# Kernel tuning notes

Measured on AMD Instinct MI355X. Metric: run time of the kernel, lower is better.

The kernel has to match this reference:

```python
import jax, jax.numpy as jnp
import numpy as np

OBS, ACT, H, B = 128, 32, 64, 32768
TMAX = 8  # max variable-length GRU steps: (15-1)//2+1 == 15//2+1 == 8
CENTER = 7


def gru_last(x_seq, valid, Wih, Whh, bih, bhh):
    """torch nn.GRU cell, masked scan; returns final hidden at each true length.
    x_seq: (B, TMAX, D), valid: (B, TMAX) bool. Gate order r, z, n."""
    Bn = x_seq.shape[0]
    h0 = jnp.zeros((Bn, Whh.shape[1]), x_seq.dtype)

    def step(h, inp):
        xt, vt = inp  # (B, D), (B,)
        gi = xt @ Wih.T + bih
        gh = h @ Whh.T + bhh
        ir, iz, inn = jnp.split(gi, 3, axis=-1)
        hr, hz, hn = jnp.split(gh, 3, axis=-1)
        r = jax.nn.sigmoid(ir + hr)
        zg = jax.nn.sigmoid(iz + hz)
        n = jnp.tanh(inn + r * hn)
        hnew = (1.0 - zg) * n + zg * h
        h = jnp.where(vt[:, None], hnew, h)
        return h, None

    h, _ = jax.lax.scan(step, h0, (jnp.swapaxes(x_seq, 0, 1), valid.T))
    return h


def setup_inputs() -> dict:
    key = jax.random.key(0)
    ks = jax.random.split(key, 20)
    def p(k, shape, s=0.05):
        return jax.random.normal(k, shape, jnp.float32) * s
    D = OBS + ACT
    return dict(
        obs_chunk=jax.random.normal(ks[0], (B, 15, OBS), jnp.float32),
        act_chunk=jax.random.normal(ks[1], (B, 15, ACT), jnp.float32),
        ln_g=jnp.ones((3,), jnp.float32), ln_b=jnp.zeros((3,), jnp.float32),
        dw1=p(ks[2], (16, 3)), db1=jnp.zeros((16,), jnp.float32),
        dw2=p(ks[3], (8, 16)), db2=jnp.zeros((8,), jnp.float32),
        dw3=p(ks[4], (14, 8)), db3=jnp.zeros((14,), jnp.float32),
        Wih_f=p(ks[5], (3 * H, D)), Whh_f=p(ks[6], (3 * H, H)),
        bih_f=jnp.zeros((3 * H,), jnp.float32), bhh_f=jnp.zeros((3 * H,), jnp.float32),
        Wih_b=p(ks[7], (3 * H, D)), Whh_b=p(ks[8], (3 * H, H)),
        bih_b=jnp.zeros((3 * H,), jnp.float32), bhh_b=jnp.zeros((3 * H,), jnp.float32),
        mw1=p(ks[9], (H, 2 * H)), mb1=jnp.zeros((H,), jnp.float32),
        mw2=p(ks[10], (H, H)), mb2=jnp.zeros((H,), jnp.float32),
        mu_w=p(ks[11], (H, H)), mu_b=jnp.zeros((H,), jnp.float32),
        lv_w=p(ks[12], (H, H)), lv_b=jnp.zeros((H,), jnp.float32),
    )


def reference(obs_chunk, act_chunk, ln_g, ln_b, dw1, db1, dw2, db2, dw3, db3,
              Wih_f, Whh_f, bih_f, bhh_f, Wih_b, Whh_b, bih_b, bhh_b,
              mw1, mb1, mw2, mb2, mu_w, mu_b, lv_w, lv_b):
    C = CENTER
    # --- DynamicTimeWindow features ---
    obs_t = obs_chunk[:, C]  # (B, OBS)
    pr = jax.nn.softmax(obs_t, axis=-1)
    entropy = -jnp.sum(pr * jnp.log(pr + 1e-8), axis=-1, keepdims=True)
    diffs = jnp.stack([jnp.linalg.norm(obs_chunk[:, C - k] - obs_chunk[:, C - k - 1], axis=-1)
                       for k in range(3)], axis=1)
    roc = diffs.mean(axis=1, keepdims=True)
    act_prev = act_chunk[:, C - 1]
    md = max(obs_t.shape[-1], act_prev.shape[-1])
    op = jnp.pad(obs_t, ((0, 0), (0, md - obs_t.shape[-1])))
    ap = jnp.pad(act_prev, ((0, 0), (0, md - act_prev.shape[-1])))
    oc = op - op.mean(axis=1, keepdims=True)
    ac = ap - ap.mean(axis=1, keepdims=True)
    denom = (jnp.linalg.norm(oc, axis=1, keepdims=True)
             * jnp.linalg.norm(ac, axis=1, keepdims=True) + 1e-8)
    corr = jnp.sum(oc * ac, axis=1, keepdims=True) / denom
    f = jnp.concatenate([entropy, roc, corr], axis=1)  # (B, 3)
    mean = f.mean(axis=-1, keepdims=True)
    var = f.var(axis=-1, keepdims=True)  # biased, matches torch LayerNorm
    fn = (f - mean) / jnp.sqrt(var + 1e-5) * ln_g + ln_b
    h1 = jax.nn.relu(fn @ dw1.T + db1)
    h2 = jax.nn.relu(h1 @ dw2.T + db2)
    logits = h2 @ dw3.T + db3  # (B, 14)
    widx = jnp.argmax(logits, axis=1)  # test_mode: argmax of softmax == argmax of logits
    wl = widx + 2  # window_len in [2, 15]
    idxs = jnp.arange(15)[None, :]
    start = (C - (wl - 1) // 2)[:, None]
    end = (C + wl // 2 + 1)[:, None]
    mask = ((idxs >= start) & (idxs < end)).astype(obs_chunk.dtype)  # (B, 15)
    x = jnp.concatenate([obs_chunk, act_chunk], axis=-1) * mask[..., None]  # (B, 15, D)
    # --- BiGRU over variable-length windows ---
    len_f = (wl - 1) // 2 + 1  # (B,)
    len_b = wl // 2 + 1
    t = jnp.arange(TMAX)
    idx_f = C - len_f[:, None] + 1 + t[None, :]  # left-aligned forward window
    idx_b = C + len_b[:, None] - 1 - t[None, :]  # reversed backward window
    seq_f = jnp.take_along_axis(x, idx_f[..., None], axis=1)  # (B, 8, D)
    seq_b = jnp.take_along_axis(x, idx_b[..., None], axis=1)
    vf = t[None, :] < len_f[:, None]
    vb = t[None, :] < len_b[:, None]
    h_f = gru_last(seq_f, vf, Wih_f, Whh_f, bih_f, bhh_f)  # (B, H)
    h_b = gru_last(seq_b, vb, Wih_b, Whh_b, bih_b, bhh_b)
    comb = jnp.concatenate([h_f, h_b], axis=1)  # (B, 2H)
    zenc = jax.nn.relu(comb @ mw1.T + mb1) @ mw2.T + mb2
    mu = zenc @ mu_w.T + mu_b
    sigma = jnp.exp(0.5 * (zenc @ lv_w.T + lv_b))
    z = mu  # test_mode=True
    return (z, mu, sigma)
```

## Files before the change

### kernel.cpp

```cpp
#include <hip/hip_runtime.h>

#define OBS 128
#define ACTD 32
#define DIMX 160
#define HID 64
#define NBATCH 32768
#define TMAXX 8
#define CTR 7
#define NPOS 15

typedef short bf16x8 __attribute__((ext_vector_type(8)));
typedef float f32x4 __attribute__((ext_vector_type(4)));

#define MFMA(a,b,c) __builtin_amdgcn_mfma_f32_16x16x32_bf16((a),(b),(c),0,0,0)

#define CTRL_BYTE 262144
#define SIDX_BYTE 278528
#define SIDX_CAP  66048
#define WB_BYTE   542720
#define COMB_BYTE 755712
#define NCB 64
#define EPB 512
#define BB_OFF 40
#define BH_OFF (40 + 1024)
#define HEAD_W_OFF 10752
#define TOTAL_SLOTS 13312

__device__ __forceinline__ unsigned short f2bf(float f) {
  unsigned u = __float_as_uint(f);
  return (unsigned short)((u + 0x7FFFu + ((u >> 16) & 1u)) >> 16);
}
__device__ __forceinline__ unsigned cvtpk(float a, float b) {
  unsigned r;
  asm("v_cvt_pk_bf16_f32 %0, %1, %2" : "=v"(r) : "v"(a), "v"(b));
  return r;
}

__device__ __forceinline__ float wsum(float v) {
#pragma unroll
  for (int s = 1; s < 64; s <<= 1) v += __shfl_xor(v, s);
  return v;
}
__device__ __forceinline__ float wmax(float v) {
#pragma unroll
  for (int s = 1; s < 64; s <<= 1) v = fmaxf(v, __shfl_xor(v, s));
  return v;
}

__global__ __launch_bounds__(256) void k_prep(
    const float* __restrict__ Wih_f, const float* __restrict__ Whh_f,
    const float* __restrict__ Wih_b, const float* __restrict__ Whh_b,
    const float* __restrict__ mw1, const float* __restrict__ mw2,
    const float* __restrict__ mu_w, const float* __restrict__ lv_w,
    unsigned short* __restrict__ dst) {
  int slot = blockIdx.x * 256 + threadIdx.x;
  if (slot >= TOTAL_SLOTS) return;
  const float* src;
  if (slot < HEAD_W_OFF) {
    int d = slot / 5376, r = slot % 5376;
    int f = r >> 8, rw = r & 255;
    int w = rw >> 6, lane = rw & 63;
    int col = lane & 15, kgrp = lane >> 4;
    int row = 16 * w + col;
    if (f < 15) {
      int g = f / 5, kf = f % 5;
      const float* W = d ? Wih_b : Wih_f;
      src = W + (size_t)(g * 64 + row) * 160 + kf * 32 + kgrp * 8;
    } else {
      int f2 = f - 15, g = f2 >> 1, kh = f2 & 1;
      const float* W = d ? Whh_b : Whh_f;
      src = W + (size_t)(g * 64 + row) * 64 + kh * 32 + kgrp * 8;
    }
  } else {
    int s2 = slot - HEAD_W_OFF;
    int f = s2 >> 8, rw = s2 & 255;
    int w = rw >> 6, lane = rw & 63;
    int col = lane & 15, kgrp = lane >> 4;
    int gr = 16 * w + col;
    if (f < 4)      src = mw1 + (size_t)gr * 128 + f * 32 + kgrp * 8;
    else if (f < 6) src = mw2 + (size_t)gr * 64 + (f - 4) * 32 + kgrp * 8;
    else if (f < 8) src = mu_w + (size_t)gr * 64 + (f - 6) * 32 + kgrp * 8;
    else            src = lv_w + (size_t)gr * 64 + (f - 8) * 32 + kgrp * 8;
  }
  unsigned short* o = dst + (size_t)slot * 8;
#pragma unroll
  for (int i = 0; i < 8; i++) o[i] = f2bf(src[i]);
}

__global__ __launch_bounds__(256) void k_decide(
    const float* __restrict__ obs, const float* __restrict__ act,
    const float* __restrict__ ln_g, const float* __restrict__ ln_b,
    const float* __restrict__ dw1, const float* __restrict__ db1,
    const float* __restrict__ dw2, const float* __restrict__ db2,
    const float* __restrict__ dw3, const float* __restrict__ db3,
    int* __restrict__ lens) {
  int b = blockIdx.x * 4 + (threadIdx.x >> 6);
  int l = threadIdx.x & 63;
  const float* o7 = obs + ((size_t)b * NPOS + CTR) * OBS;
  const float* o6 = o7 - OBS;
  const float* o5 = o7 - 2 * OBS;
  const float* o4 = o7 - 3 * OBS;
  float x0 = o7[l], x1 = o7[l + 64];
  float y60 = o6[l], y61 = o6[l + 64];
  float y50 = o5[l], y51 = o5[l + 64];
  float y40 = o4[l], y41 = o4[l + 64];
  float ap = (l < 32) ? act[((size_t)b * NPOS + 6) * ACTD + l] : 0.0f;

  float m = wmax(fmaxf(x0, x1));
  float e0 = __expf(x0 - m), e1 = __expf(x1 - m);
  float s = wsum(e0 + e1);
  float dot = wsum(e0 * (x0 - m) + e1 * (x1 - m));
  float ent = __logf(s) - dot / s;

  float d0 = wsum((x0 - y60) * (x0 - y60) + (x1 - y61) * (x1 - y61));
  float d1 = wsum((y60 - y50) * (y60 - y50) + (y61 - y51) * (y61 - y51));
  float d2 = wsum((y50 - y40) * (y50 - y40) + (y51 - y41) * (y51 - y41));
  float roc = (sqrtf(d0) + sqrtf(d1) + sqrtf(d2)) / 3.0f;

  float sop = wsum(x0 + x1);
  float sop2 = wsum(x0 * x0 + x1 * x1);
  float sap = wsum(ap);
  float sap2 = wsum(ap * ap);
  float dotoa = wsum(ap * x0);
  float mo = sop / 128.0f, ma = sap / 128.0f;
  float num = dotoa - 128.0f * mo * ma;
  float oc2 = fmaxf(sop2 - 128.0f * mo * mo, 0.0f);
  float ac2 = fmaxf(sap2 - 128.0f * ma * ma, 0.0f);
  float corr = num / (sqrtf(oc2) * sqrtf(ac2) + 1e-8f);

  float f0 = ent, f1 = roc, f2 = corr;
  float mean = (f0 + f1 + f2) / 3.0f;
  float v0 = f0 - mean, v1 = f1 - mean, v2 = f2 - mean;
  float var = (v0 * v0 + v1 * v1 + v2 * v2) / 3.0f;
  float sd = sqrtf(var + 1e-5f);
  float fn0 = v0 / sd * ln_g[0] + ln_b[0];
  float fn1 = v1 / sd * ln_g[1] + ln_b[1];
  float fn2 = v2 / sd * ln_g[2] + ln_b[2];

  float h1[16];
#pragma unroll
  for (int i = 0; i < 16; i++) {
    float a = db1[i] + fn0 * dw1[i * 3] + fn1 * dw1[i * 3 + 1] + fn2 * dw1[i * 3 + 2];
    h1[i] = fmaxf(a, 0.0f);
  }
  float h2[8];
#pragma unroll
  for (int i = 0; i < 8; i++) {
    float a = db2[i];
#pragma unroll
    for (int j = 0; j < 16; j++) a += h1[j] * dw2[i * 16 + j];
    h2[i] = fmaxf(a, 0.0f);
  }
  float best = -3.0e38f;
  int bi = 0;
#pragma unroll
  for (int i = 0; i < 14; i++) {
    float a = db3[i];
#pragma unroll
    for (int j = 0; j < 8; j++) a += h2[j] * dw3[i * 8 + j];
    if (a > best) { best = a; bi = i; }
  }
  int wl = bi + 2;
  if (l == 0) {
    lens[b] = (wl - 1) / 2 + 1;
    lens[NBATCH + b] = wl / 2 + 1;
  }
}

__global__ __launch_bounds__(256) void k_count(
    const int* __restrict__ lens, int* __restrict__ ctrl) {
  __shared__ int hist[16];
  const int tid = threadIdx.x, blk = blockIdx.x;
  if (tid < 16) hist[tid] = 0;
  __syncthreads();
#pragma unroll
  for (int j = 0; j < 2; j++) {
    int e = blk * EPB + j * 256 + tid;
    atomicAdd(&hist[lens[e] - 1], 1);
    atomicAdd(&hist[8 + lens[NBATCH + e] - 1], 1);
  }
  __syncthreads();
  if (tid < 16) ctrl[BH_OFF + blk * 16 + tid] = hist[tid];
}

__global__ void k_scan(int* __restrict__ ctrl, int* __restrict__ sidx) {
  __shared__ int tot[16];
  __shared__ int pss[17];
  __shared__ int border[16];
  __shared__ int bstart[16];
  const int tid = threadIdx.x;
  const int* bh = ctrl + BH_OFF;
  int* bb = ctrl + BB_OFF;
  if (tid < 16) {
    int s = 0;
    for (int blk = 0; blk < NCB; blk++) {
      bb[blk * 16 + tid] = s;
      s += bh[blk * 16 + tid];
    }
    tot[tid] = s;
  }
  __syncthreads();
  if (tid == 0) {
    int acc = 0;
    for (int r = 0; r < 16; r++) {
      int bin = (r & 1) * 8 + 7 - (r >> 1);
      border[r] = bin;
      pss[r] = acc;
      bstart[bin] = acc;
      acc += (tot[bin] + 31) & ~31;
    }
    pss[16] = acc;
    for (int r = 0; r < 17; r++) ctrl[r] = pss[r];
    for (int r = 0; r < 16; r++) ctrl[17 + r] = border[r];
  }
  __syncthreads();
  if (tid < 16) {
    for (int blk = 0; blk < NCB; blk++) bb[blk * 16 + tid] += bstart[tid];
  }
  __syncthreads();
  for (int r = 0; r < 16; r++) {
    int bin = border[r];
    int s = pss[r] + tot[bin], e2 = pss[r + 1];
    for (int i = s + tid; i < e2; i += 64) sidx[i] = -1;
  }
}

__global__ __launch_bounds__(256) void k_place(
    const int* __restrict__ lens, const int* __restrict__ ctrl,
    int* __restrict__ sidx) {
  __shared__ int hist[16];
  __shared__ int base[16];
  const int tid = threadIdx.x, blk = blockIdx.x;
  if (tid < 16) {
    hist[tid] = 0;
    base[tid] = ctrl[BB_OFF + blk * 16 + tid];
  }
  __syncthreads();
#pragma unroll
  for (int j = 0; j < 2; j++) {
    int e = blk * EPB + j * 256 + tid;
    int binf = lens[e] - 1;
    sidx[base[binf] + atomicAdd(&hist[binf], 1)] = e;
    int binb = 8 + lens[NBATCH + e] - 1;
    sidx[base[binb] + atomicAdd(&hist[binb], 1)] = e;
  }
}

__global__ __launch_bounds__(256, 2) void k_gru(
    const float* __restrict__ obs, const float* __restrict__ act,
    const int* __restrict__ ctrl, const int* __restrict__ sidx,
    const unsigned short* __restrict__ wbf,
    const float* __restrict__ bih_f, const float* __restrict__ bhh_f,
    const float* __restrict__ bih_b, const float* __restrict__ bhh_b,
    unsigned short* __restrict__ comb) {
  __shared__ unsigned short Xl[2][32 * 168];
  __shared__ unsigned short Hl[2][32 * 72];
  __shared__ int ei[32];

  const int tid = threadIdx.x;
  const int p = blockIdx.x * 32;
  if (p >= ctrl[16]) return;
  int r = 0;
#pragma unroll
  for (int k = 1; k < 16; k++) r += (p >= ctrl[k]) ? 1 : 0;
  const int bin = ctrl[17 + r];
  const int d = bin >> 3;
  const int len = (bin & 7) + 1;

  if (tid < 32) ei[tid] = sidx[p + tid];
  __syncthreads();

  const int w = tid >> 6, l = tid & 63;
  const int col = l & 15, kgrp = l >> 4;
  const int gr = 16 * w + col;

  const float* bih = d ? bih_b : bih_f;
  const float* bhh = d ? bhh_b : bhh_f;
  const float bias_r = bih[gr] + bhh[gr];
  const float bias_z = bih[64 + gr] + bhh[64 + gr];
  const float bias_in = bih[128 + gr];
  const float bias_hn = bhh[128 + gr];

  const unsigned short* fb = wbf + ((size_t)d * 5376 + tid) * 8;
  bf16x8 wr[5], wz[5], wn[5];
#pragma unroll
  for (int kf = 0; kf < 5; kf++) {
    wr[kf] = *(const bf16x8*)(fb + (size_t)kf * 2048);
    wz[kf] = *(const bf16x8*)(fb + (size_t)(5 + kf) * 2048);
    wn[kf] = *(const bf16x8*)(fb + (size_t)(10 + kf) * 2048);
  }
  bf16x8 vr[2], vz[2], vn[2];
#pragma unroll
  for (int kh = 0; kh < 2; kh++) {
    vr[kh] = *(const bf16x8*)(fb + (size_t)(15 + kh) * 2048);
    vz[kh] = *(const bf16x8*)(fb + (size_t)(17 + kh) * 2048);
    vn[kh] = *(const bf16x8*)(fb + (size_t)(19 + kh) * 2048);
  }

  const int p0 = d ? (CTR + len - 1) : (CTR - len + 1);
  const float* pst[5];
  int sstr[5], sdo[5];
#pragma unroll
  for (int it = 0; it < 5; it++) {
    int i = tid + it * 256;
    int eloc = i / 40;
    int q = i - eloc * 40;
    int eg = ei[eloc];
    if (eg < 0) eg = ei[0];
    if (q < 32) {
      pst[it] = obs + ((size_t)eg * NPOS + p0) * OBS + q * 4;
      sstr[it] = d ? -OBS : OBS;
    } else {
      pst[it] = act + ((size_t)eg * NPOS + p0) * ACTD + (q - 32) * 4;
      sstr[it] = d ? -ACTD : ACTD;
    }
    sdo[it] = eloc * 168 + ((q < 32) ? q * 4 : 128 + (q - 32) * 4);
  }
  float4 sv[5];

  auto stage_issue = [&](int t1) {
#pragma unroll
    for (int it = 0; it < 5; it++)
      sv[it] = *(const float4*)(pst[it] + (ptrdiff_t)t1 * sstr[it]);
  };
  auto stage_commit = [&](int buf) {
#pragma unroll
    for (int it = 0; it < 5; it++) {
      uint2 pk;
      pk.x = cvtpk(sv[it].x, sv[it].y);
      pk.y = cvtpk(sv[it].z, sv[it].w);
      *(uint2*)(&Xl[buf][sdo[it]]) = pk;
    }
  };

  stage_issue(0);
  stage_commit(0);
  __syncthreads();

  f32x4 hreg[2];
#pragma unroll
  for (int m = 0; m < 2; m++) hreg[m] = (f32x4){0.f, 0.f, 0.f, 0.f};

  for (int t = 0; t < len; t++) {
    const int cur = t & 1, nxt = cur ^ 1;
    const bool more = (t + 1 < len);
    if (more) stage_issue(t + 1);

    f32x4 ar[2], az[2], ain[2], ahn[2];
#pragma unroll
    for (int m = 0; m < 2; m++) {
      ar[m] = (f32x4){0.f, 0.f, 0.f, 0.f};
      az[m] = (f32x4){0.f, 0.f, 0.f, 0.f};
      ain[m] = (f32x4){0.f, 0.f, 0.f, 0.f};
      ahn[m] = (f32x4){0.f, 0.f, 0.f, 0.f};
    }
#pragma unroll
    for (int kf = 0; kf < 5; kf++) {
#pragma unroll
      for (int m = 0; m < 2; m++) {
        bf16x8 xa = *(const bf16x8*)(&Xl[cur][(col + 16 * m) * 168 + kf * 32 + kgrp * 8]);
        ar[m] = MFMA(xa, wr[kf], ar[m]);
        az[m] = MFMA(xa, wz[kf], az[m]);
        ain[m] = MFMA(xa, wn[kf], ain[m]);
      }
    }
    if (t > 0) {
#pragma unroll
      for (int kh = 0; kh < 2; kh++) {
#pragma unroll
        for (int m = 0; m < 2; m++) {
          bf16x8 ha = *(const bf16x8*)(&Hl[cur][(col + 16 * m) * 72 + kh * 32 + kgrp * 8]);
          ar[m] = MFMA(ha, vr[kh], ar[m]);
          az[m] = MFMA(ha, vz[kh], az[m]);
          ahn[m] = MFMA(ha, vn[kh], ahn[m]);
        }
      }
    }

#pragma unroll
    for (int m = 0; m < 2; m++) {
      float hvv[4];
#pragma unroll
      for (int r2 = 0; r2 < 4; r2++) {
        float air = ar[m][r2] + bias_r;
        float aiz = az[m][r2] + bias_z;
        float rg = __builtin_amdgcn_rcpf(1.0f + __expf(-air));
        float zg = __builtin_amdgcn_rcpf(1.0f + __expf(-aiz));
        float nn = fmaf(rg, ahn[m][r2] + bias_hn, ain[m][r2] + bias_in);
        float th = fmaf(-2.0f, __builtin_amdgcn_rcpf(__expf(2.0f * nn) + 1.0f), 1.0f);
        float hp = hreg[m][r2];
        float hv = fmaf(zg, hp - th, th);
        hreg[m][r2] = hv;
        hvv[r2] = hv;
      }
      if (more) {
        unsigned ua = cvtpk(hvv[0], hvv[1]);
        unsigned ub = cvtpk(hvv[2], hvv[3]);
        int row0 = (16 * m + kgrp * 4) * 72 + gr;
        Hl[nxt][row0] = (unsigned short)ua;
        Hl[nxt][row0 + 72] = (unsigned short)(ua >> 16);
        Hl[nxt][row0 + 144] = (unsigned short)ub;
        Hl[nxt][row0 + 216] = (unsigned short)(ub >> 16);
      }
    }

    if (more) {
      stage_commit(nxt);
      __syncthreads();
    }
  }

#pragma unroll
  for (int m = 0; m < 2; m++) {
#pragma unroll
    for (int r2 = 0; r2 < 4; r2++) {
      int eg = ei[16 * m + kgrp * 4 + r2];
      if (eg >= 0)
        comb[(size_t)eg * 128 + 64 * d + gr] = f2bf(hreg[m][r2]);
    }
  }
}

__global__ __launch_bounds__(256) void k_head(
    const unsigned short* __restrict__ comb, const unsigned short* __restrict__ wbf,
    const float* __restrict__ mb1, const float* __restrict__ mb2,
    const float* __restrict__ mu_b, const float* __restrict__ lv_b,
    float* __restrict__ out) {
  __shared__ unsigned short Cl[64 * 136];
  __shared__ unsigned short Hl[64 * 72];
  __shared__ unsigned short Zl[64 * 72];

  const int tid = threadIdx.x;
  const int w = tid >> 6, l = tid & 63;
  const int col = l & 15, kgrp = l >> 4;
  const int gr = 16 * w + col;
  const int base = blockIdx.x * 64;

  {
    int row = tid >> 2, sq = tid & 3;
    const uint4* src = (const uint4*)(comb + (size_t)(base + row) * 128 + sq * 32);
    uint4* dst = (uint4*)(&Cl[row * 136 + sq * 32]);
#pragma unroll
    for (int j = 0; j < 4; j++) dst[j] = src[j];
  }
  __syncthreads();

  const unsigned short* hfb = wbf + ((size_t)HEAD_W_OFF + tid) * 8;
  const float b1 = mb1[gr], b2v = mb2[gr], bmu = mu_b[gr], blv = lv_b[gr];

  f32x4 t1[4];
#pragma unroll
  for (int m = 0; m < 4; m++) t1[m] = (f32x4){0.f, 0.f, 0.f, 0.f};
#pragma unroll
  for (int kf = 0; kf < 4; kf++) {
    bf16x8 bw = *(const bf16x8*)(hfb + (size_t)kf * 2048);
#pragma unroll
    for (int m = 0; m < 4; m++) {
      bf16x8 ca = *(const bf16x8*)(&Cl[(col + 16 * m) * 136 + kf * 32 + kgrp * 8]);
      t1[m] = MFMA(ca, bw, t1[m]);
    }
  }
#pragma unroll
  for (int m = 0; m < 4; m++) {
#pragma unroll
    for (int r = 0; r < 4; r++) {
      float v = fmaxf(t1[m][r] + b1, 0.0f);
      Hl[(16 * m + kgrp * 4 + r) * 72 + gr] = f2bf(v);
    }
  }
  __syncthreads();

  f32x4 ze[4];
#pragma unroll
  for (int m = 0; m < 4; m++) ze[m] = (f32x4){0.f, 0.f, 0.f, 0.f};
#pragma unroll
  for (int kh = 0; kh < 2; kh++) {
    bf16x8 bw = *(const bf16x8*)(hfb + (size_t)(4 + kh) * 2048);
#pragma unroll
    for (int m = 0; m < 4; m++) {
      bf16x8 ha = *(const bf16x8*)(&Hl[(col + 16 * m) * 72 + kh * 32 + kgrp * 8]);
      ze[m] = MFMA(ha, bw, ze[m]);
    }
  }
#pragma unroll
  for (int m = 0; m < 4; m++) {
#pragma unroll
    for (int r = 0; r < 4; r++) {
      Zl[(16 * m + kgrp * 4 + r) * 72 + gr] = f2bf(ze[m][r] + b2v);
    }
  }
  __syncthreads();

  f32x4 amu[4], alv[4];
#pragma unroll
  for (int m = 0; m < 4; m++) {
    amu[m] = (f32x4){0.f, 0.f, 0.f, 0.f};
    alv[m] = (f32x4){0.f, 0.f, 0.f, 0.f};
  }
#pragma unroll
  for (int kh = 0; kh < 2; kh++) {
    bf16x8 bwm = *(const bf16x8*)(hfb + (size_t)(6 + kh) * 2048);
    bf16x8 bwl = *(const bf16x8*)(hfb + (size_t)(8 + kh) * 2048);
#pragma unroll
    for (int m = 0; m < 4; m++) {
      bf16x8 za = *(const bf16x8*)(&Zl[(col + 16 * m) * 72 + kh * 32 + kgrp * 8]);
      amu[m] = MFMA(za, bwm, amu[m]);
      alv[m] = MFMA(za, bwl, alv[m]);
    }
  }
#pragma unroll
  for (int m = 0; m < 4; m++) {
#pragma unroll
    for (int r = 0; r < 4; r++) {
      int e = 16 * m + kgrp * 4 + r;
      float mu = amu[m][r] + bmu;
      float sg = expf(0.5f * (alv[m][r] + blv));
      size_t o = (size_t)(base + e) * HID + gr;
      out[o] = mu;
      out[(size_t)NBATCH * HID + o] = mu;
      out[2 * (size_t)NBATCH * HID + o] = sg;
    }
  }
}

extern "C" void kernel_launch(void* const* d_in, const int* in_sizes, int n_in,
                              void* d_out, int out_size, void* d_ws, size_t ws_size,
                              hipStream_t stream) {
  const float* obs = (const float*)d_in[0];
  const float* act = (const float*)d_in[1];
  const float* ln_g = (const float*)d_in[2];
  const float* ln_b = (const float*)d_in[3];
  const float* dw1 = (const float*)d_in[4];
  const float* db1 = (const float*)d_in[5];
  const float* dw2 = (const float*)d_in[6];
  const float* db2 = (const float*)d_in[7];
  const float* dw3 = (const float*)d_in[8];
  const float* db3 = (const float*)d_in[9];
  const float* Wih_f = (const float*)d_in[10];
  const float* Whh_f = (const float*)d_in[11];
  const float* bih_f = (const float*)d_in[12];
  const float* bhh_f = (const float*)d_in[13];
  const float* Wih_b = (const float*)d_in[14];
  const float* Whh_b = (const float*)d_in[15];
  const float* bih_b = (const float*)d_in[16];
  const float* bhh_b = (const float*)d_in[17];
  const float* mw1 = (const float*)d_in[18];
  const float* mb1 = (const float*)d_in[19];
  const float* mw2 = (const float*)d_in[20];
  const float* mb2 = (const float*)d_in[21];
  const float* mu_w = (const float*)d_in[22];
  const float* mu_b = (const float*)d_in[23];
  const float* lv_w = (const float*)d_in[24];
  const float* lv_b = (const float*)d_in[25];

  int* lens = (int*)d_ws;
  int* ctrl = (int*)((char*)d_ws + CTRL_BYTE);
  int* sidx = (int*)((char*)d_ws + SIDX_BYTE);
  unsigned short* wbf = (unsigned short*)((char*)d_ws + WB_BYTE);
  unsigned short* comb = (unsigned short*)((char*)d_ws + COMB_BYTE);

  k_prep<<<(TOTAL_SLOTS + 255) / 256, 256, 0, stream>>>(
      Wih_f, Whh_f, Wih_b, Whh_b, mw1, mw2, mu_w, lv_w, wbf);
  k_decide<<<NBATCH / 4, 256, 0, stream>>>(obs, act, ln_g, ln_b, dw1, db1, dw2,
                                           db2, dw3, db3, lens);
  k_count<<<NCB, 256, 0, stream>>>(lens, ctrl);
  k_scan<<<1, 64, 0, stream>>>(ctrl, sidx);
  k_place<<<NCB, 256, 0, stream>>>(lens, ctrl, sidx);
  k_gru<<<SIDX_CAP / 32, 256, 0, stream>>>(obs, act, ctrl, sidx, wbf, bih_f,
                                           bhh_f, bih_b, bhh_b, comb);
  k_head<<<NBATCH / 64, 256, 0, stream>>>(comb, wbf, mb1, mb2, mu_b, lv_b,
                                          (float*)d_out);
}
```

Before: 125.8 us.

## Fuse weight prep into count kernel, merge scan with place, fold biases into accumulators

Folds the bf16 weight-packing work into the histogram-count kernel (64 blocks × 208 slots covers all 13312 slots). It also merges the single-block scan kernel with the placement kernel, so each block recomputes its own prefix redundantly. Together these cut the pipeline from seven launches to five and remove a serial single-block step. In the GRU loop, the accumulators now start at the bias values instead of zero, which removes per-element bias adds. The cost is redundant prefix work in every block, plus extra memory traffic inside the count kernel.

```diff
diff --git a/kernel.cpp b/kernel.cpp
--- a/kernel.cpp
+++ b/kernel.cpp
@@ -21,7 +21,6 @@
 #define COMB_BYTE 755712
 #define NCB 64
 #define EPB 512
-#define BB_OFF 40
 #define BH_OFF (40 + 1024)
 #define HEAD_W_OFF 10752
 #define TOTAL_SLOTS 13312
@@ -45,46 +44,6 @@
 #pragma unroll
   for (int s = 1; s < 64; s <<= 1) v = fmaxf(v, __shfl_xor(v, s));
   return v;
-}
-
-__global__ __launch_bounds__(256) void k_prep(
-    const float* __restrict__ Wih_f, const float* __restrict__ Whh_f,
-    const float* __restrict__ Wih_b, const float* __restrict__ Whh_b,
-    const float* __restrict__ mw1, const float* __restrict__ mw2,
-    const float* __restrict__ mu_w, const float* __restrict__ lv_w,
-    unsigned short* __restrict__ dst) {
-  int slot = blockIdx.x * 256 + threadIdx.x;
-  if (slot >= TOTAL_SLOTS) return;
-  const float* src;
-  if (slot < HEAD_W_OFF) {
-    int d = slot / 5376, r = slot % 5376;
-    int f = r >> 8, rw = r & 255;
-    int w = rw >> 6, lane = rw & 63;
-    int col = lane & 15, kgrp = lane >> 4;
-    int row = 16 * w + col;
-    if (f < 15) {
-      int g = f / 5, kf = f % 5;
-      const float* W = d ? Wih_b : Wih_f;
-      src = W + (size_t)(g * 64 + row) * 160 + kf * 32 + kgrp * 8;
-    } else {
-      int f2 = f - 15, g = f2 >> 1, kh = f2 & 1;
-      const float* W = d ? Whh_b : Whh_f;
-      src = W + (size_t)(g * 64 + row) * 64 + kh * 32 + kgrp * 8;
-    }
-  } else {
-    int s2 = slot - HEAD_W_OFF;
-    int f = s2 >> 8, rw = s2 & 255;
-    int w = rw >> 6, lane = rw & 63;
-    int col = lane & 15, kgrp = lane >> 4;
-    int gr = 16 * w + col;
-    if (f < 4)      src = mw1 + (size_t)gr * 128 + f * 32 + kgrp * 8;
-    else if (f < 6) src = mw2 + (size_t)gr * 64 + (f - 4) * 32 + kgrp * 8;
-    else if (f < 8) src = mu_w + (size_t)gr * 64 + (f - 6) * 32 + kgrp * 8;
-    else            src = lv_w + (size_t)gr * 64 + (f - 8) * 32 + kgrp * 8;
-  }
-  unsigned short* o = dst + (size_t)slot * 8;
-#pragma unroll
-  for (int i = 0; i < 8; i++) o[i] = f2bf(src[i]);
 }
 
 __global__ __launch_bounds__(256) void k_decide(
@@ -167,8 +126,13 @@
   }
 }
 
-__global__ __launch_bounds__(256) void k_count(
-    const int* __restrict__ lens, int* __restrict__ ctrl) {
+__global__ __launch_bounds__(256) void k_cp(
+    const int* __restrict__ lens, int* __restrict__ ctrl,
+    const float* __restrict__ Wih_f, const float* __restrict__ Whh_f,
+    const float* __restrict__ Wih_b, const float* __restrict__ Whh_b,
+    const float* __restrict__ mw1, const float* __restrict__ mw2,
+    const float* __restrict__ mu_w, const float* __restrict__ lv_w,
+    unsigned short* __restrict__ dst) {
   __shared__ int hist[16];
   const int tid = threadIdx.x, blk = blockIdx.x;
   if (tid < 16) hist[tid] = 0;
@@ -179,25 +143,67 @@
     atomicAdd(&hist[lens[e] - 1], 1);
     atomicAdd(&hist[8 + lens[NBATCH + e] - 1], 1);
   }
+  {
+    int slot = blk * 208 + (tid % 208) + (tid / 208) * 13312;
+    if (tid < 208) {
+      const float* src;
+      if (slot < HEAD_W_OFF) {
+        int d = slot / 5376, r = slot % 5376;
+        int f = r >> 8, rw = r & 255;
+        int w = rw >> 6, lane = rw & 63;
+        int col = lane & 15, kgrp = lane >> 4;
+        int row = 16 * w + col;
+        if (f < 15) {
+          int g = f / 5, kf = f % 5;
+          const float* W = d ? Wih_b : Wih_f;
+          src = W + (size_t)(g * 64 + row) * 160 + kf * 32 + kgrp * 8;
+        } else {
+          int f2 = f - 15, g = f2 >> 1, kh = f2 & 1;
+          const float* W = d ? Whh_b : Whh_f;
+          src = W + (size_t)(g * 64 + row) * 64 + kh * 32 + kgrp * 8;
+        }
+      } else {
+        int s2 = slot - HEAD_W_OFF;
+        int f = s2 >> 8, rw = s2 & 255;
+        int w = rw >> 6, lane = rw & 63;
+        int col = lane & 15, kgrp = lane >> 4;
+        int gr = 16 * w + col;
+        if (f < 4)      src = mw1 + (size_t)gr * 128 + f * 32 + kgrp * 8;
+        else if (f < 6) src = mw2 + (size_t)gr * 64 + (f - 4) * 32 + kgrp * 8;
+        else if (f < 8) src = mu_w + (size_t)gr * 64 + (f - 6) * 32 + kgrp * 8;
+        else            src = lv_w + (size_t)gr * 64 + (f - 8) * 32 + kgrp * 8;
+      }
+      unsigned short* o = dst + (size_t)slot * 8;
+#pragma unroll
+      for (int i = 0; i < 8; i++) o[i] = f2bf(src[i]);
+    }
+  }
   __syncthreads();
   if (tid < 16) ctrl[BH_OFF + blk * 16 + tid] = hist[tid];
 }
 
-__global__ void k_scan(int* __restrict__ ctrl, int* __restrict__ sidx) {
+__global__ __launch_bounds__(256) void k_scanplace(
+    const int* __restrict__ lens, int* __restrict__ ctrl,
+    int* __restrict__ sidx) {
+  __shared__ int hist[16];
+  __shared__ int base[16];
   __shared__ int tot[16];
+  __shared__ int pre[16];
   __shared__ int pss[17];
   __shared__ int border[16];
   __shared__ int bstart[16];
-  const int tid = threadIdx.x;
+  const int tid = threadIdx.x, blk = blockIdx.x;
   const int* bh = ctrl + BH_OFF;
-  int* bb = ctrl + BB_OFF;
   if (tid < 16) {
-    int s = 0;
-    for (int blk = 0; blk < NCB; blk++) {
-      bb[blk * 16 + tid] = s;
-      s += bh[blk * 16 + tid];
-    }
-    tot[tid] = s;
+    int t = 0, pr = 0;
+    for (int b2 = 0; b2 < NCB; b2++) {
+      int h = bh[b2 * 16 + tid];
+      if (b2 < blk) pr += h;
+      t += h;
+    }
+    tot[tid] = t;
+    pre[tid] = pr;
+    hist[tid] = 0;
   }
   __syncthreads();
   if (tid == 0) {
@@ -210,32 +216,21 @@
       acc += (tot[bin] + 31) & ~31;
     }
     pss[16] = acc;
-    for (int r = 0; r < 17; r++) ctrl[r] = pss[r];
-    for (int r = 0; r < 16; r++) ctrl[17 + r] = border[r];
-  }
-  __syncthreads();
-  if (tid < 16) {
-    for (int blk = 0; blk < NCB; blk++) bb[blk * 16 + tid] += bstart[tid];
-  }
-  __syncthreads();
-  for (int r = 0; r < 16; r++) {
-    int bin = border[r];
-    int s = pss[r] + tot[bin], e2 = pss[r + 1];
-    for (int i = s + tid; i < e2; i += 64) sidx[i] = -1;
-  }
-}
-
-__global__ __launch_bounds__(256) void k_place(
-    const int* __restrict__ lens, const int* __restrict__ ctrl,
-    int* __restrict__ sidx) {
-  __shared__ int hist[16];
-  __shared__ int base[16];
-  const int tid = threadIdx.x, blk = blockIdx.x;
-  if (tid < 16) {
-    hist[tid] = 0;
-    base[tid] = ctrl[BB_OFF + blk * 16 + tid];
-  }
-  __syncthreads();
+    if (blk == 0) {
+      for (int r = 0; r < 17; r++) ctrl[r] = pss[r];
+      for (int r = 0; r < 16; r++) ctrl[17 + r] = border[r];
+    }
+  }
+  __syncthreads();
+  if (tid < 16) base[tid] = bstart[tid] + pre[tid];
+  __syncthreads();
+  if (blk == 0) {
+    for (int r = 0; r < 16; r++) {
+      int bin = border[r];
+      int s = pss[r] + tot[bin], e2 = pss[r + 1];
+      for (int i = s + tid; i < e2; i += 256) sidx[i] = -1;
+    }
+  }
 #pragma unroll
   for (int j = 0; j < 2; j++) {
     int e = blk * EPB + j * 256 + tid;
@@ -349,10 +344,10 @@
     f32x4 ar[2], az[2], ain[2], ahn[2];
 #pragma unroll
     for (int m = 0; m < 2; m++) {
-      ar[m] = (f32x4){0.f, 0.f, 0.f, 0.f};
-      az[m] = (f32x4){0.f, 0.f, 0.f, 0.f};
-      ain[m] = (f32x4){0.f, 0.f, 0.f, 0.f};
-      ahn[m] = (f32x4){0.f, 0.f, 0.f, 0.f};
+      ar[m] = (f32x4){bias_r, bias_r, bias_r, bias_r};
+      az[m] = (f32x4){bias_z, bias_z, bias_z, bias_z};
+      ain[m] = (f32x4){bias_in, bias_in, bias_in, bias_in};
+      ahn[m] = (f32x4){bias_hn, bias_hn, bias_hn, bias_hn};
     }
 #pragma unroll
     for (int kf = 0; kf < 5; kf++) {
@@ -382,11 +377,9 @@
       float hvv[4];
 #pragma unroll
       for (int r2 = 0; r2 < 4; r2++) {
-        float air = ar[m][r2] + bias_r;
-        float aiz = az[m][r2] + bias_z;
-        float rg = __builtin_amdgcn_rcpf(1.0f + __expf(-air));
-        float zg = __builtin_amdgcn_rcpf(1.0f + __expf(-aiz));
-        float nn = fmaf(rg, ahn[m][r2] + bias_hn, ain[m][r2] + bias_in);
+        float rg = __builtin_amdgcn_rcpf(1.0f + __expf(-ar[m][r2]));
+        float zg = __builtin_amdgcn_rcpf(1.0f + __expf(-az[m][r2]));
+        float nn = fmaf(rg, ahn[m][r2], ain[m][r2]);
         float th = fmaf(-2.0f, __builtin_amdgcn_rcpf(__expf(2.0f * nn) + 1.0f), 1.0f);
         float hp = hreg[m][r2];
         float hv = fmaf(zg, hp - th, th);
@@ -559,13 +552,11 @@
   unsigned short* wbf = (unsigned short*)((char*)d_ws + WB_BYTE);
   unsigned short* comb = (unsigned short*)((char*)d_ws + COMB_BYTE);
 
-  k_prep<<<(TOTAL_SLOTS + 255) / 256, 256, 0, stream>>>(
-      Wih_f, Whh_f, Wih_b, Whh_b, mw1, mw2, mu_w, lv_w, wbf);
   k_decide<<<NBATCH / 4, 256, 0, stream>>>(obs, act, ln_g, ln_b, dw1, db1, dw2,
                                            db2, dw3, db3, lens);
-  k_count<<<NCB, 256, 0, stream>>>(lens, ctrl);
-  k_scan<<<1, 64, 0, stream>>>(ctrl, sidx);
-  k_place<<<NCB, 256, 0, stream>>>(lens, ctrl, sidx);
+  k_cp<<<NCB, 256, 0, stream>>>(lens, ctrl, Wih_f, Whh_f, Wih_b, Whh_b, mw1,
+                                mw2, mu_w, lv_w, wbf);
+  k_scanplace<<<NCB, 256, 0, stream>>>(lens, ctrl, sidx);
   k_gru<<<SIDX_CAP / 32, 256, 0, stream>>>(obs, act, ctrl, sidx, wbf, bih_f,
                                            bhh_f, bih_b, bhh_b, comb);
   k_head<<<NBATCH / 64, 256, 0, stream>>>(comb, wbf, mb1, mb2, mu_b, lv_b,
```

New measurement: 112.9 us. 10.3% less time.
